# Performance work log

Hardware: AMD Instinct MI355X
Metric: run time of the kernel (lower is better)

Reference implementation:

```python
import jax, jax.numpy as jnp
import numpy as np

B_, S_, D_, N_ = 4, 2048, 1024, 16

def setup_inputs() -> dict:
    key = jax.random.key(0)
    ks = jax.random.split(key, 8)
    x = jax.random.normal(ks[0], (B_, S_, D_), dtype=jnp.float32)
    A = jax.random.normal(ks[1], (D_, N_, N_), dtype=jnp.float32) * 0.1
    Bm = jax.random.normal(ks[2], (D_, N_), dtype=jnp.float32) * 0.1
    Cm = jax.random.normal(ks[3], (D_, N_), dtype=jnp.float32) * 0.1
    Dm = jax.random.normal(ks[4], (D_,), dtype=jnp.float32) * 0.1
    ln_w = jnp.ones((D_,), dtype=jnp.float32)
    ln_b = jnp.zeros((D_,), dtype=jnp.float32)
    W_out = jax.random.normal(ks[5], (D_, D_), dtype=jnp.float32) * (1.0 / np.sqrt(D_))
    b_out = jnp.zeros((D_,), dtype=jnp.float32)
    return {"x": x, "A": A, "Bm": Bm, "Cm": Cm, "Dm": Dm,
            "ln_w": ln_w, "ln_b": ln_b, "W_out": W_out, "b_out": b_out}

def _layernorm(y, w, b, eps=1e-5):
    mu = jnp.mean(y, axis=-1, keepdims=True)
    var = jnp.mean((y - mu) ** 2, axis=-1, keepdims=True)
    return (y - mu) * jax.lax.rsqrt(var + eps) * w + b

def reference(x, A, Bm, Cm, Dm, ln_w, ln_b, W_out, b_out):
    # x: [B, S, D]; per-channel SSM: h_t = A h_{t-1} + B x_t ; y_t = C.h_t + D x_t
    bsz = x.shape[0]
    h0 = jnp.zeros((bsz, A.shape[0], A.shape[1]), dtype=x.dtype)  # [B, D, N]

    def step(h, x_t):  # x_t: [B, D]
        h = jnp.einsum('dnm,bdm->bdn', A, h) + Bm[None] * x_t[..., None]
        y_t = jnp.einsum('dn,bdn->bd', Cm, h) + Dm * x_t
        return h, y_t

    _, y = jax.lax.scan(step, h0, jnp.swapaxes(x, 0, 1))  # y: [S, B, D]
    y = jnp.swapaxes(y, 0, 1)  # [B, S, D]
    y = _layernorm(y, ln_w, ln_b)
    y = jax.nn.gelu(y, approximate=False)
    y = y @ W_out.T + b_out
    return x + y
```

## Files before the change

### kernel.cpp

```cpp
#include <hip/hip_runtime.h>
#include <hip/hip_bf16.h>

#define D_DIM 1024
#define S_DIM 2048
#define B_DIM 4
#define KTAPS 16

typedef short bf16x8 __attribute__((ext_vector_type(8)));
typedef float f32x4 __attribute__((ext_vector_type(4)));

#define GLOAD16(gptr, lptr) \
  __builtin_amdgcn_global_load_lds((const __attribute__((address_space(1))) unsigned int*)(gptr), \
                                   (__attribute__((address_space(3))) unsigned int*)(lptr), 16, 0, 0)

#define WAIT_VM0 0x0F70

static __device__ __forceinline__ short f2bs(float f) {
  __hip_bfloat16 h = __float2bfloat16(f);
  return *reinterpret_cast<short*>(&h);
}
static __device__ __forceinline__ float bs2f(short s) {
  unsigned int u = ((unsigned int)(unsigned short)s) << 16;
  return __builtin_bit_cast(float, u);
}

__global__ void setup_kernel(const float* __restrict__ W, __hip_bfloat16* __restrict__ Wbf,
                             const float* __restrict__ A, const float* __restrict__ Bm,
                             const float* __restrict__ Cm, const float* __restrict__ Dm,
                             float* __restrict__ gT) {
  if (blockIdx.x < 4096) {
    const int f    = blockIdx.x * 256 + threadIdx.x;
    const int p    = f >> 14;
    const int k0   = (f >> 9) & 31;
    const int lane = (f >> 3) & 63;
    const int j    = f & 7;
    const int n    = p * 16 + (lane & 15);
    const int k    = k0 * 32 + (lane >> 4) * 8 + j;
    Wbf[f] = __float2bfloat16(W[n * D_DIM + k]);
    return;
  }
  const int gb   = blockIdx.x - 4096;
  const int wid  = threadIdx.x >> 6;
  const int lane = threadIdx.x & 63;
  const int sub  = lane >> 4;
  const int n    = lane & 15;
  const int d    = gb * 16 + wid * 4 + sub;
  float Ar[16];
#pragma unroll
  for (int m = 0; m < 16; ++m) Ar[m] = A[d * 256 + n * 16 + m];
  float v = Bm[d * 16 + n];
  const float c   = Cm[d * 16 + n];
  const float dmv = Dm[d];
  const int base  = sub << 4;
  for (int k = 0; k < KTAPS; ++k) {
    float dot = c * v;
    dot += __shfl_xor(dot, 1);
    dot += __shfl_xor(dot, 2);
    dot += __shfl_xor(dot, 4);
    dot += __shfl_xor(dot, 8);
    if (k == 0) dot += dmv;
    if (n == 0) gT[k * D_DIM + d] = dot;
    float nv = 0.f;
#pragma unroll
    for (int m = 0; m < 16; ++m) nv = fmaf(Ar[m], __shfl(v, base + m), nv);
    v = nv;
  }
}

__global__ __launch_bounds__(256, 4) void conv_kernel(const float* __restrict__ x,
                                                      const float* __restrict__ gT,
                                                      __hip_bfloat16* __restrict__ y) {
  const int bx    = blockIdx.x;
  const int b     = bx >> 7;
  const int rem   = bx & 127;
  const int chunk = rem >> 2;
  const int dg    = rem & 3;
  const int d     = dg * 256 + threadIdx.x;
  const int s0    = chunk * 64;
  const float* xb = x + b * (S_DIM * D_DIM) + d;
  short* yb       = (short*)y + b * (S_DIM * D_DIM) + d;

  float g[KTAPS];
#pragma unroll
  for (int k = 0; k < KTAPS; ++k) g[k] = gT[k * D_DIM + d];

  float hist[16];
#pragma unroll
  for (int i = 0; i < 16; ++i) {
    int s = s0 - 16 + i;
    hist[i] = (s >= 0) ? xb[s * D_DIM] : 0.0f;
  }

  for (int t = 0; t < 4; ++t) {
    const int sb = s0 + t * 16;
    float cur[16];
#pragma unroll
    for (int i = 0; i < 16; ++i) cur[i] = xb[(sb + i) * D_DIM];
#pragma unroll
    for (int j = 0; j < 16; ++j) {
      float acc = 0.f;
#pragma unroll
      for (int k = 0; k < KTAPS; ++k) {
        const int idx = j - k;
        const float xv = (idx >= 0) ? cur[idx] : hist[16 + idx];
        acc = fmaf(g[k], xv, acc);
      }
      yb[(sb + j) * D_DIM] = f2bs(acc);
    }
#pragma unroll
    for (int i = 0; i < 16; ++i) hist[i] = cur[i];
  }
}

__global__ __launch_bounds__(256) void ln_gelu_kernel(const __hip_bfloat16* __restrict__ y,
                                                      const float* __restrict__ w,
                                                      const float* __restrict__ bsh,
                                                      __hip_bfloat16* __restrict__ act) {
  __shared__ float red0[4];
  __shared__ float red1[4];
  const int row = blockIdx.x;
  const int tid = threadIdx.x;
  const int lane = tid & 63, wid = tid >> 6;
  const int d0 = tid * 4;

  const short4 s4 = *(const short4*)((const short*)y + (size_t)row * D_DIM + d0);
  float v[4] = {bs2f(s4.x), bs2f(s4.y), bs2f(s4.z), bs2f(s4.w)};

  float s = v[0] + v[1] + v[2] + v[3];
  s += __shfl_xor(s, 1);  s += __shfl_xor(s, 2);  s += __shfl_xor(s, 4);
  s += __shfl_xor(s, 8);  s += __shfl_xor(s, 16); s += __shfl_xor(s, 32);
  if (lane == 0) red0[wid] = s;
  __syncthreads();
  const float mu = (red0[0] + red0[1] + red0[2] + red0[3]) * (1.0f / D_DIM);

  float sq = 0.f;
#pragma unroll
  for (int j = 0; j < 4; ++j) { float t = v[j] - mu; sq = fmaf(t, t, sq); }
  sq += __shfl_xor(sq, 1);  sq += __shfl_xor(sq, 2);  sq += __shfl_xor(sq, 4);
  sq += __shfl_xor(sq, 8);  sq += __shfl_xor(sq, 16); sq += __shfl_xor(sq, 32);
  if (lane == 0) red1[wid] = sq;
  __syncthreads();
  const float var = (red1[0] + red1[1] + red1[2] + red1[3]) * (1.0f / D_DIM);
  const float inv = rsqrtf(var + 1e-5f);

  const float4 w4 = *(const float4*)&w[d0];
  const float4 b4 = *(const float4*)&bsh[d0];
  const float wv[4] = {w4.x, w4.y, w4.z, w4.w};
  const float bv[4] = {b4.x, b4.y, b4.z, b4.w};
  short4 o;
  short* op = &o.x;
#pragma unroll
  for (int j = 0; j < 4; ++j) {
    float t = (v[j] - mu) * inv * wv[j] + bv[j];
    float ge = 0.5f * t * (1.f + erff(t * 0.70710678118654752f));
    op[j] = f2bs(ge);
  }
  *(short4*)((short*)act + (size_t)row * D_DIM + d0) = o;
}

__global__ __launch_bounds__(256, 2) void gemm_kernel(const __hip_bfloat16* __restrict__ Act,
                                                      const __hip_bfloat16* __restrict__ Wbf,
                                                      const float* __restrict__ x,
                                                      const float* __restrict__ bout,
                                                      float* __restrict__ out) {
  __shared__ short Al[2][128 * 128];
  const int tid  = threadIdx.x;
  const int lane = tid & 63;
  const int wave = tid >> 6;
  const int mBase = blockIdx.x * 128;
  const int nBase = blockIdx.y * 128;
  const int wm = (wave & 1) * 64;
  const int wn = (wave >> 1) * 64;
  const int l16 = lane & 15;
  const int kq  = lane >> 4;

  const int srow = tid >> 4;
  const int cg   = (tid & 15) ^ (srow & 7);
  const short* Ag = (const short*)Act + (mBase + srow) * D_DIM + cg * 8;

  const short* Bf = (const short*)Wbf + lane * 8;

  f32x4 acc[4][4];
#pragma unroll
  for (int mt = 0; mt < 4; ++mt)
#pragma unroll
    for (int nt = 0; nt < 4; ++nt) acc[mt][nt] = (f32x4){0.f, 0.f, 0.f, 0.f};

#pragma unroll
  for (int r = 0; r < 8; ++r)
    GLOAD16(Ag + r * 16 * D_DIM, &Al[0][tid * 8 + r * 2048]);

  const int pnW = (nBase + wn) >> 4;

  for (int it = 0; it < 8; ++it) {
    const int cur = it & 1;
    __builtin_amdgcn_s_waitcnt(WAIT_VM0);
    __builtin_amdgcn_s_barrier();
    if (it < 7) {
      const int k1 = (it + 1) * 128;
#pragma unroll
      for (int r = 0; r < 8; ++r)
        GLOAD16(Ag + r * 16 * D_DIM + k1, &Al[cur ^ 1][tid * 8 + r * 2048]);
    }
    const short* Ab = Al[cur];
#pragma unroll
    for (int kki = 0; kki < 4; ++kki) {
      const int kk = kki * 32;
      const int k0_32 = it * 4 + kki;
      bf16x8 af[4], bfr[4];
#pragma unroll
      for (int nt = 0; nt < 4; ++nt)
        bfr[nt] = *(const bf16x8*)(Bf + (((size_t)(pnW + nt) * 32 + k0_32) << 9));
      const int cgr = (kk >> 3) + kq;
#pragma unroll
      for (int mt = 0; mt < 4; ++mt) {
        const int r = wm + mt * 16 + l16;
        af[mt] = *(const bf16x8*)&Ab[r * 128 + ((cgr ^ (r & 7)) << 3)];
      }
#pragma unroll
      for (int mt = 0; mt < 4; ++mt)
#pragma unroll
        for (int nt = 0; nt < 4; ++nt)
          acc[mt][nt] = __builtin_amdgcn_mfma_f32_16x16x32_bf16(af[mt], bfr[nt], acc[mt][nt], 0, 0, 0);
    }
  }

  const int r0 = kq * 4;
#pragma unroll
  for (int mt = 0; mt < 4; ++mt) {
    const int row = mBase + wm + mt * 16 + r0;
#pragma unroll
    for (int nt = 0; nt < 4; ++nt) {
      const int col = nBase + wn + nt * 16 + l16;
      const float bo = bout[col];
#pragma unroll
      for (int r = 0; r < 4; ++r) {
        const int idx = (row + r) * D_DIM + col;
        out[idx] = x[idx] + acc[mt][nt][r] + bo;
      }
    }
  }
}

extern "C" void kernel_launch(void* const* d_in, const int* in_sizes, int n_in,
                              void* d_out, int out_size, void* d_ws, size_t ws_size,
                              hipStream_t stream) {
  const float* x    = (const float*)d_in[0];
  const float* A    = (const float*)d_in[1];
  const float* Bm   = (const float*)d_in[2];
  const float* Cm   = (const float*)d_in[3];
  const float* Dm   = (const float*)d_in[4];
  const float* lnw  = (const float*)d_in[5];
  const float* lnb  = (const float*)d_in[6];
  const float* Wout = (const float*)d_in[7];
  const float* bout = (const float*)d_in[8];
  float* out = (float*)d_out;

  char* ws = (char*)d_ws;
  float* gT            = (float*)ws;
  __hip_bfloat16* Wbf  = (__hip_bfloat16*)(ws + 262144);
  __hip_bfloat16* Act  = (__hip_bfloat16*)(ws + 2359296);
  __hip_bfloat16* ybf  = (__hip_bfloat16*)(ws + 19136512);

  setup_kernel<<<4160, 256, 0, stream>>>(Wout, Wbf, A, Bm, Cm, Dm, gT);
  conv_kernel<<<512, 256, 0, stream>>>(x, gT, ybf);
  ln_gelu_kernel<<<8192, 256, 0, stream>>>(ybf, lnw, lnb, Act);
  gemm_kernel<<<dim3(64, 8), 256, 0, stream>>>(Act, Wbf, x, bout, out);
}
```

Before: 172.6 us.

## Write activations in MFMA fragment layout and drop LDS staging in GEMM

The LayerNorm+GELU kernel now handles 8 elements per thread and writes its bf16 output straight into the pre-swizzled MFMA fragment layout already used for the weights. The GEMM becomes a single-wave 64x64 tile kernel that loads both operands directly from global memory as contiguous 16-byte fragments, with no LDS double buffering or barriers. This removes the LDS traffic and synchronisation, but A-fragment reuse now relies on cache rather than shared memory. Each 64x64 tile reloads its operands, so global and L2 traffic rises.

```diff
diff --git a/kernel.cpp b/kernel.cpp
--- a/kernel.cpp
+++ b/kernel.cpp
@@ -9,12 +9,6 @@
 typedef short bf16x8 __attribute__((ext_vector_type(8)));
 typedef float f32x4 __attribute__((ext_vector_type(4)));
 
-#define GLOAD16(gptr, lptr) \
-  __builtin_amdgcn_global_load_lds((const __attribute__((address_space(1))) unsigned int*)(gptr), \
-                                   (__attribute__((address_space(3))) unsigned int*)(lptr), 16, 0, 0)
-
-#define WAIT_VM0 0x0F70
-
 static __device__ __forceinline__ short f2bs(float f) {
   __hip_bfloat16 h = __float2bfloat16(f);
   return *reinterpret_cast<short*>(&h);
@@ -23,6 +17,7 @@
   unsigned int u = ((unsigned int)(unsigned short)s) << 16;
   return __builtin_bit_cast(float, u);
 }
+
 
 __global__ void setup_kernel(const float* __restrict__ W, __hip_bfloat16* __restrict__ Wbf,
                              const float* __restrict__ A, const float* __restrict__ Bm,
@@ -112,73 +107,75 @@
   }
 }
 
-__global__ __launch_bounds__(256) void ln_gelu_kernel(const __hip_bfloat16* __restrict__ y,
+__global__ __launch_bounds__(128) void ln_gelu_kernel(const __hip_bfloat16* __restrict__ y,
                                                       const float* __restrict__ w,
                                                       const float* __restrict__ bsh,
                                                       __hip_bfloat16* __restrict__ act) {
-  __shared__ float red0[4];
-  __shared__ float red1[4];
+  __shared__ float red0[2];
+  __shared__ float red1[2];
   const int row = blockIdx.x;
   const int tid = threadIdx.x;
   const int lane = tid & 63, wid = tid >> 6;
-  const int d0 = tid * 4;
-
-  const short4 s4 = *(const short4*)((const short*)y + (size_t)row * D_DIM + d0);
-  float v[4] = {bs2f(s4.x), bs2f(s4.y), bs2f(s4.z), bs2f(s4.w)};
-
-  float s = v[0] + v[1] + v[2] + v[3];
+  const int kb = tid * 8;
+
+  const bf16x8 s8 = *(const bf16x8*)((const short*)y + (size_t)row * D_DIM + kb);
+  float v[8];
+#pragma unroll
+  for (int j = 0; j < 8; ++j) v[j] = bs2f(s8[j]);
+
+  float s = 0.f;
+#pragma unroll
+  for (int j = 0; j < 8; ++j) s += v[j];
   s += __shfl_xor(s, 1);  s += __shfl_xor(s, 2);  s += __shfl_xor(s, 4);
   s += __shfl_xor(s, 8);  s += __shfl_xor(s, 16); s += __shfl_xor(s, 32);
   if (lane == 0) red0[wid] = s;
   __syncthreads();
-  const float mu = (red0[0] + red0[1] + red0[2] + red0[3]) * (1.0f / D_DIM);
+  const float mu = (red0[0] + red0[1]) * (1.0f / D_DIM);
 
   float sq = 0.f;
 #pragma unroll
-  for (int j = 0; j < 4; ++j) { float t = v[j] - mu; sq = fmaf(t, t, sq); }
+  for (int j = 0; j < 8; ++j) { float t = v[j] - mu; sq = fmaf(t, t, sq); }
   sq += __shfl_xor(sq, 1);  sq += __shfl_xor(sq, 2);  sq += __shfl_xor(sq, 4);
   sq += __shfl_xor(sq, 8);  sq += __shfl_xor(sq, 16); sq += __shfl_xor(sq, 32);
   if (lane == 0) red1[wid] = sq;
   __syncthreads();
-  const float var = (red1[0] + red1[1] + red1[2] + red1[3]) * (1.0f / D_DIM);
+  const float var = (red1[0] + red1[1]) * (1.0f / D_DIM);
   const float inv = rsqrtf(var + 1e-5f);
 
-  const float4 w4 = *(const float4*)&w[d0];
-  const float4 b4 = *(const float4*)&bsh[d0];
-  const float wv[4] = {w4.x, w4.y, w4.z, w4.w};
-  const float bv[4] = {b4.x, b4.y, b4.z, b4.w};
-  short4 o;
-  short* op = &o.x;
-#pragma unroll
-  for (int j = 0; j < 4; ++j) {
+  const float4 w0 = *(const float4*)&w[kb];
+  const float4 w1 = *(const float4*)&w[kb + 4];
+  const float4 b0 = *(const float4*)&bsh[kb];
+  const float4 b1 = *(const float4*)&bsh[kb + 4];
+  const float wv[8] = {w0.x, w0.y, w0.z, w0.w, w1.x, w1.y, w1.z, w1.w};
+  const float bv[8] = {b0.x, b0.y, b0.z, b0.w, b1.x, b1.y, b1.z, b1.w};
+  bf16x8 o;
+#pragma unroll
+  for (int j = 0; j < 8; ++j) {
     float t = (v[j] - mu) * inv * wv[j] + bv[j];
     float ge = 0.5f * t * (1.f + erff(t * 0.70710678118654752f));
-    op[j] = f2bs(ge);
-  }
-  *(short4*)((short*)act + (size_t)row * D_DIM + d0) = o;
-}
-
-__global__ __launch_bounds__(256, 2) void gemm_kernel(const __hip_bfloat16* __restrict__ Act,
-                                                      const __hip_bfloat16* __restrict__ Wbf,
-                                                      const float* __restrict__ x,
-                                                      const float* __restrict__ bout,
-                                                      float* __restrict__ out) {
-  __shared__ short Al[2][128 * 128];
-  const int tid  = threadIdx.x;
-  const int lane = tid & 63;
-  const int wave = tid >> 6;
-  const int mBase = blockIdx.x * 128;
-  const int nBase = blockIdx.y * 128;
-  const int wm = (wave & 1) * 64;
-  const int wn = (wave >> 1) * 64;
-  const int l16 = lane & 15;
-  const int kq  = lane >> 4;
-
-  const int srow = tid >> 4;
-  const int cg   = (tid & 15) ^ (srow & 7);
-  const short* Ag = (const short*)Act + (mBase + srow) * D_DIM + cg * 8;
-
-  const short* Bf = (const short*)Wbf + lane * 8;
+    o[j] = f2bs(ge);
+  }
+  const int p    = row >> 4;
+  const int k0   = tid >> 2;
+  const int sub  = tid & 3;
+  const int flane = sub * 16 + (row & 15);
+  const size_t f = (((size_t)(p * 32 + k0) * 64) + flane) * 8;
+  *(bf16x8*)((short*)act + f) = o;
+}
+
+__global__ __launch_bounds__(64, 2) void gemm_kernel(const __hip_bfloat16* __restrict__ Actf,
+                                                     const __hip_bfloat16* __restrict__ Wbf,
+                                                     const float* __restrict__ x,
+                                                     const float* __restrict__ bout,
+                                                     float* __restrict__ out) {
+  const int lane = threadIdx.x;
+  const int mt64 = blockIdx.x & 127;
+  const int nt64 = blockIdx.x >> 7;
+  const int l16  = lane & 15;
+  const int kq   = lane >> 4;
+
+  const short* Af = (const short*)Actf + ((size_t)mt64 * 4) * 16384 + lane * 8;
+  const short* Bf = (const short*)Wbf  + ((size_t)nt64 * 4) * 16384 + lane * 8;
 
   f32x4 acc[4][4];
 #pragma unroll
@@ -186,52 +183,29 @@
 #pragma unroll
     for (int nt = 0; nt < 4; ++nt) acc[mt][nt] = (f32x4){0.f, 0.f, 0.f, 0.f};
 
-#pragma unroll
-  for (int r = 0; r < 8; ++r)
-    GLOAD16(Ag + r * 16 * D_DIM, &Al[0][tid * 8 + r * 2048]);
-
-  const int pnW = (nBase + wn) >> 4;
-
-  for (int it = 0; it < 8; ++it) {
-    const int cur = it & 1;
-    __builtin_amdgcn_s_waitcnt(WAIT_VM0);
-    __builtin_amdgcn_s_barrier();
-    if (it < 7) {
-      const int k1 = (it + 1) * 128;
-#pragma unroll
-      for (int r = 0; r < 8; ++r)
-        GLOAD16(Ag + r * 16 * D_DIM + k1, &Al[cur ^ 1][tid * 8 + r * 2048]);
-    }
-    const short* Ab = Al[cur];
-#pragma unroll
-    for (int kki = 0; kki < 4; ++kki) {
-      const int kk = kki * 32;
-      const int k0_32 = it * 4 + kki;
-      bf16x8 af[4], bfr[4];
+#pragma unroll 2
+  for (int k0 = 0; k0 < 32; ++k0) {
+    bf16x8 a[4], b[4];
+#pragma unroll
+    for (int mt = 0; mt < 4; ++mt)
+      a[mt] = *(const bf16x8*)(Af + ((size_t)(mt * 32 + k0) << 9));
+#pragma unroll
+    for (int nt = 0; nt < 4; ++nt)
+      b[nt] = *(const bf16x8*)(Bf + ((size_t)(nt * 32 + k0) << 9));
+#pragma unroll
+    for (int mt = 0; mt < 4; ++mt)
 #pragma unroll
       for (int nt = 0; nt < 4; ++nt)
-        bfr[nt] = *(const bf16x8*)(Bf + (((size_t)(pnW + nt) * 32 + k0_32) << 9));
-      const int cgr = (kk >> 3) + kq;
-#pragma unroll
-      for (int mt = 0; mt < 4; ++mt) {
-        const int r = wm + mt * 16 + l16;
-        af[mt] = *(const bf16x8*)&Ab[r * 128 + ((cgr ^ (r & 7)) << 3)];
-      }
-#pragma unroll
-      for (int mt = 0; mt < 4; ++mt)
-#pragma unroll
-        for (int nt = 0; nt < 4; ++nt)
-          acc[mt][nt] = __builtin_amdgcn_mfma_f32_16x16x32_bf16(af[mt], bfr[nt], acc[mt][nt], 0, 0, 0);
-    }
+        acc[mt][nt] = __builtin_amdgcn_mfma_f32_16x16x32_bf16(a[mt], b[nt], acc[mt][nt], 0, 0, 0);
   }
 
   const int r0 = kq * 4;
 #pragma unroll
   for (int mt = 0; mt < 4; ++mt) {
-    const int row = mBase + wm + mt * 16 + r0;
+    const int row = mt64 * 64 + mt * 16 + r0;
 #pragma unroll
     for (int nt = 0; nt < 4; ++nt) {
-      const int col = nBase + wn + nt * 16 + l16;
+      const int col = nt64 * 64 + nt * 16 + l16;
       const float bo = bout[col];
 #pragma unroll
       for (int r = 0; r < 4; ++r) {
@@ -259,11 +233,11 @@
   char* ws = (char*)d_ws;
   float* gT            = (float*)ws;
   __hip_bfloat16* Wbf  = (__hip_bfloat16*)(ws + 262144);
-  __hip_bfloat16* Act  = (__hip_bfloat16*)(ws + 2359296);
+  __hip_bfloat16* Actf = (__hip_bfloat16*)(ws + 2359296);
   __hip_bfloat16* ybf  = (__hip_bfloat16*)(ws + 19136512);
 
   setup_kernel<<<4160, 256, 0, stream>>>(Wout, Wbf, A, Bm, Cm, Dm, gT);
   conv_kernel<<<512, 256, 0, stream>>>(x, gT, ybf);
-  ln_gelu_kernel<<<8192, 256, 0, stream>>>(ybf, lnw, lnb, Act);
-  gemm_kernel<<<dim3(64, 8), 256, 0, stream>>>(Act, Wbf, x, bout, out);
-}
+  ln_gelu_kernel<<<8192, 128, 0, stream>>>(ybf, lnw, lnb, Actf);
+  gemm_kernel<<<2048, 64, 0, stream>>>(Actf, Wbf, x, bout, out);
+}
```

New measurement: 175.8 us. Within noise of the previous version (+1.8%).
